# Kernel optimization log

Hardware: AMD Instinct MI355X
Metric: run time of the kernel (lower is better)

Reference implementation:

```python
import jax, jax.numpy as jnp
import numpy as np

TEMP = 0.7
EPS = 1e-6
LN_EPS = 1e-5
CAP_FACTOR = 2.0


def setup_inputs() -> dict:
    key = jax.random.key(0)
    B, S, H, E = 8, 4096, 2048, 8
    H2 = H // 2
    ks = jax.random.split(key, 3)
    x = jax.random.normal(ks[0], (B, S, H), jnp.float32)
    ln_w = jnp.ones((H,), jnp.float32)
    ln_b = jnp.zeros((H,), jnp.float32)
    # kaiming_normal_(fan_in, relu): std = sqrt(2 / fan_in)
    w1 = jax.random.normal(ks[1], (H2, H), jnp.float32) * np.float32(np.sqrt(2.0 / H))
    b1 = jnp.zeros((H2,), jnp.float32)
    w2 = jax.random.normal(ks[2], (E, H2), jnp.float32) * np.float32(np.sqrt(2.0 / H2))
    b2 = jnp.zeros((E,), jnp.float32)
    return {"x": x, "ln_w": ln_w, "ln_b": ln_b, "w1": w1, "b1": b1,
            "w2": w2, "b2": b2, "top_k": 2, "num_experts": E}


def _forward(x, ln_w, ln_b, w1, b1, w2, b2, top_k, num_experts):
    B, S, H = x.shape
    N = B * S
    # router: LayerNorm -> Linear -> GELU(exact) -> Linear
    mu = x.mean(-1, keepdims=True)
    var = jnp.mean((x - mu) ** 2, axis=-1, keepdims=True)
    h = (x - mu) * jax.lax.rsqrt(var + LN_EPS) * ln_w + ln_b
    h = jax.nn.gelu(h @ w1.T + b1, approximate=False)
    logits = h @ w2.T + b2
    ew = jnp.clip(logits / TEMP, -50.0, 50.0)  # [B,S,E]

    flat = ew.reshape(N, num_experts)
    capacity = int(CAP_FACTOR * N * top_k / num_experts)

    # top-k per token + softmax over the k selected logits, scatter into dense mask
    tk_w, tk_i = jax.lax.top_k(flat, top_k)          # [N,k]
    sm = jax.nn.softmax(tk_w, axis=-1)               # [N,k]
    rows = jnp.arange(N)[:, None]
    masks = jnp.zeros((N, num_experts), flat.dtype).at[rows, tk_i].set(sm)

    # capacity drop: per expert column, if sum of weights > capacity keep only
    # the top-`capacity` weighted tokens (extra zero-valued picks are no-ops,
    # matching the torch min(capacity, nnz) behavior).
    cols = masks.T                                   # [E,N]
    sums = cols.sum(-1)                              # [E]
    kcap = min(capacity, N)
    tv, ti = jax.lax.top_k(cols, kcap)               # [E,kcap]
    erow = jnp.arange(num_experts)[:, None]
    capped = jnp.zeros_like(cols).at[erow, ti].set(tv)
    over = sums > capacity
    cols = jnp.where(over[:, None], capped, cols)
    count = jax.lax.stop_gradient(jnp.where(over, capped.sum(-1), sums))  # buffer, no grad

    masks = cols.T
    masks = masks / jnp.maximum(masks.sum(-1, keepdims=True), EPS)

    usage = count / jnp.maximum(count.sum(), EPS)
    target = jnp.full((num_experts,), 1.0 / num_experts, usage.dtype)
    # F.kl_div(log(usage), target, reduction='batchmean') with batch dim = E
    kl = jnp.sum(target * (jnp.log(target) - jnp.log(jnp.maximum(usage, EPS)))) / num_experts
    loss = 0.01 * kl
    return ew, masks.reshape(B, S, num_experts), loss, usage


def reference(x, ln_w, ln_b, w1, b1, w2, b2, top_k, num_experts):
    return _forward(x, ln_w, ln_b, w1, b1, w2, b2, top_k, num_experts)
```

## Files before the change

kernel.cpp:

```cpp
#include <hip/hip_runtime.h>
#include <math.h>

#define NTOK 32768
#define HDIM 2048
#define H2DIM 1024
#define NE 8

#define WS_MU 0
#define WS_RS 32768
#define WS_LOGITS 65536
#define WS_SUMS (65536 + 262144)
#define WS_C1 (WS_SUMS + NE)
#define WS_C2 (WS_C1 + 1024)
#define WS_W1_BYTES 1318976ull
#define WS_NEED (WS_W1_BYTES + 8388608ull)

#define OUT_MASKS 262144
#define OUT_LOSS 524288
#define OUT_USAGE 524289

typedef _Float16 half8 __attribute__((ext_vector_type(8)));
typedef float floatx16 __attribute__((ext_vector_type(16)));

#define H_SCALE 0.03125f

__global__ __launch_bounds__(256) void w1prep_kernel(
    const float* __restrict__ w1, const float* __restrict__ ln_w,
    const float* __restrict__ ln_b, _Float16* __restrict__ w1p,
    float* __restrict__ C1, float* __restrict__ C2) {
  int idx = blockIdx.x * 256 + threadIdx.x;
  int n = idx >> 6, kc = idx & 63;
  const float4* src = (const float4*)(w1 + (size_t)n * HDIM + kc * 32);
  const float4* lwp = (const float4*)(ln_w + kc * 32);
  const float4* lbp = (const float4*)(ln_b + kc * 32);
  float wv[32], lwv[32], lbv[32];
#pragma unroll
  for (int v = 0; v < 8; ++v) {
    float4 f = src[v], g = lwp[v], h = lbp[v];
    wv[v*4+0]=f.x; wv[v*4+1]=f.y; wv[v*4+2]=f.z; wv[v*4+3]=f.w;
    lwv[v*4+0]=g.x; lwv[v*4+1]=g.y; lwv[v*4+2]=g.z; lwv[v*4+3]=g.w;
    lbv[v*4+0]=h.x; lbv[v*4+1]=h.y; lbv[v*4+2]=h.z; lbv[v*4+3]=h.w;
  }
  float c1 = 0.f, c2 = 0.f;
  _Float16 hi[32], lo[32];
#pragma unroll
  for (int v = 0; v < 32; ++v) {
    float wp = wv[v] * lwv[v];
    c1 += wp;
    c2 += lbv[v] * wv[v];
    float t = wp * 32.0f;
    hi[v] = (_Float16)t;
    lo[v] = (_Float16)((t - (float)hi[v]) * 4096.0f);
  }
  _Float16* dst = w1p + (size_t)idx * 64;
#pragma unroll
  for (int c = 0; c < 4; ++c) {
    half8 h = {hi[c*8+0],hi[c*8+1],hi[c*8+2],hi[c*8+3],hi[c*8+4],hi[c*8+5],hi[c*8+6],hi[c*8+7]};
    half8 l = {lo[c*8+0],lo[c*8+1],lo[c*8+2],lo[c*8+3],lo[c*8+4],lo[c*8+5],lo[c*8+6],lo[c*8+7]};
    *(half8*)&dst[c * 8] = h;
    *(half8*)&dst[32 + c * 8] = l;
  }
  atomicAdd(&C1[n], c1);
  atomicAdd(&C2[n], c2);
}

__global__ __launch_bounds__(256) void ln_stats_kernel(const float* __restrict__ x,
                                                       float* __restrict__ ws) {
  int g = blockIdx.x * 256 + threadIdx.x;
  if (g < NTOK * NE + NE + 2048) ws[WS_LOGITS + g] = 0.0f;

  int row = blockIdx.x * 4 + (threadIdx.x >> 6);
  int lane = threadIdx.x & 63;
  const float4* p = (const float4*)(x + (size_t)row * HDIM);
  float s = 0.f, sq = 0.f;
#pragma unroll
  for (int i = 0; i < 8; ++i) {
    float4 v = p[lane + 64 * i];
    s += (v.x + v.y) + (v.z + v.w);
    sq += (v.x * v.x + v.y * v.y) + (v.z * v.z + v.w * v.w);
  }
#pragma unroll
  for (int o = 32; o > 0; o >>= 1) {
    s += __shfl_xor(s, o);
    sq += __shfl_xor(sq, o);
  }
  if (lane == 0) {
    float m = s * (1.0f / HDIM);
    float var = fmaxf(sq * (1.0f / HDIM) - m * m, 0.0f);
    ws[WS_MU + row] = m;
    ws[WS_RS + row] = 1.0f / sqrtf(var + 1e-5f);
  }
}

#define LDB 40

__global__ __launch_bounds__(256, 3) void gemm_mfma_kernel(
    const float* __restrict__ x, const _Float16* __restrict__ w1p,
    const float* __restrict__ bias1, const float* __restrict__ w2,
    const float* __restrict__ mu, const float* __restrict__ rs,
    const float* __restrict__ C1, const float* __restrict__ C2,
    float* __restrict__ logits) {
  __shared__ _Float16 Ah[128 * LDB];
  __shared__ _Float16 Al[128 * LDB];
  __shared__ _Float16 Bh[128 * LDB];
  __shared__ _Float16 Bl[128 * LDB];

  const int tid = threadIdx.x;
  const int lin = blockIdx.x;
  const int xcd = lin & 7;
  const int jj = lin >> 3;
  const int m0 = (xcd * 32 + (jj >> 3)) * 128;
  const int n0 = (jj & 7) * 128;

  const int lane = tid & 63;
  const int wid = tid >> 6;
  const int wm = wid >> 1, wn = wid & 1;
  const int fr = lane & 31, fq = lane >> 5;

  const int am = tid >> 1, ak = (tid & 1) * 16;
  const float* xrow = x + (size_t)(m0 + am) * HDIM + ak;
  const int bn = tid >> 1, bp = tid & 1;
  const _Float16* bsrc = w1p + (size_t)(n0 + bn) * 4096 + bp * 32;
  _Float16* bdst = (bp ? Bl : Bh) + bn * LDB;
  _Float16* adst_h = Ah + am * LDB + ak;
  _Float16* adst_l = Al + am * LDB + ak;

  floatx16 acc[2][2];
#pragma unroll
  for (int i = 0; i < 2; ++i)
#pragma unroll
    for (int j = 0; j < 2; ++j)
#pragma unroll
      for (int r = 0; r < 16; ++r) acc[i][j][r] = 0.f;
  floatx16 zv;
#pragma unroll
  for (int r = 0; r < 16; ++r) zv[r] = 0.f;

  float4 xr0, xr1, xr2, xr3, br0, br1, br2, br3;
  {
    const float4* xp = (const float4*)xrow;
    xr0 = xp[0]; xr1 = xp[1]; xr2 = xp[2]; xr3 = xp[3];
    const float4* bq = (const float4*)bsrc;
    br0 = bq[0]; br1 = bq[1]; br2 = bq[2]; br3 = bq[3];
  }

  for (int kc = 0; kc < 64; ++kc) {
    float xa[16] = {xr0.x,xr0.y,xr0.z,xr0.w, xr1.x,xr1.y,xr1.z,xr1.w,
                    xr2.x,xr2.y,xr2.z,xr2.w, xr3.x,xr3.y,xr3.z,xr3.w};
    _Float16 hi[16], lo[16];
#pragma unroll
    for (int v = 0; v < 16; ++v) {
      hi[v] = (_Float16)xa[v];
      lo[v] = (_Float16)((xa[v] - (float)hi[v]) * 4096.0f);
    }

    __syncthreads();
    {
      half8 h0 = {hi[0],hi[1],hi[2],hi[3],hi[4],hi[5],hi[6],hi[7]};
      half8 h1 = {hi[8],hi[9],hi[10],hi[11],hi[12],hi[13],hi[14],hi[15]};
      half8 l0 = {lo[0],lo[1],lo[2],lo[3],lo[4],lo[5],lo[6],lo[7]};
      half8 l1 = {lo[8],lo[9],lo[10],lo[11],lo[12],lo[13],lo[14],lo[15]};
      *(half8*)adst_h = h0;
      *(half8*)(adst_h + 8) = h1;
      *(half8*)adst_l = l0;
      *(half8*)(adst_l + 8) = l1;
      float4* bd = (float4*)bdst;
      bd[0] = br0; bd[1] = br1; bd[2] = br2; bd[3] = br3;
    }
    __syncthreads();

    if (kc < 63) {
      const float4* xp = (const float4*)(xrow + (kc + 1) * 32);
      xr0 = xp[0]; xr1 = xp[1]; xr2 = xp[2]; xr3 = xp[3];
      const float4* bq = (const float4*)(bsrc + (size_t)(kc + 1) * 64);
      br0 = bq[0]; br1 = bq[1]; br2 = bq[2]; br3 = bq[3];
    }

#pragma unroll
    for (int t = 0; t < 2; ++t) {
      half8 ah[2], al[2], bh[2], bl[2];
#pragma unroll
      for (int i = 0; i < 2; ++i) {
        int off = (wm * 64 + i * 32 + fr) * LDB + t * 16 + fq * 8;
        ah[i] = *(const half8*)&Ah[off];
        al[i] = *(const half8*)&Al[off];
      }
#pragma unroll
      for (int j = 0; j < 2; ++j) {
        int off = (wn * 64 + j * 32 + fr) * LDB + t * 16 + fq * 8;
        bh[j] = *(const half8*)&Bh[off];
        bl[j] = *(const half8*)&Bl[off];
      }
#pragma unroll
      for (int i = 0; i < 2; ++i)
#pragma unroll
        for (int j = 0; j < 2; ++j) {
          acc[i][j] = __builtin_amdgcn_mfma_f32_32x32x16_f16(ah[i], bh[j], acc[i][j], 0, 0, 0);
          floatx16 tmp = __builtin_amdgcn_mfma_f32_32x32x16_f16(ah[i], bl[j], zv, 0, 0, 0);
          tmp = __builtin_amdgcn_mfma_f32_32x32x16_f16(al[i], bh[j], tmp, 0, 0, 0);
          acc[i][j] += tmp * (1.0f / 4096.0f);
        }
    }
  }

  const float inv_sqrt2 = 0.70710678118654752440f;
  const int c = fr;
  const int col0 = n0 + wn * 64 + c;
  const int col1 = col0 + 32;
  float w2r0[NE], w2r1[NE];
#pragma unroll
  for (int e = 0; e < NE; ++e) {
    w2r0[e] = w2[e * H2DIM + col0];
    w2r1[e] = w2[e * H2DIM + col1];
  }
  const float c1a = C1[col0], c1b = C1[col1];
  const float hb0 = C2[col0] + bias1[col0];
  const float hb1 = C2[col1] + bias1[col1];

#pragma unroll
  for (int i = 0; i < 2; ++i)
#pragma unroll
    for (int r = 0; r < 16; ++r) {
      int row = m0 + wm * 64 + i * 32 + (r & 3) + 8 * (r >> 2) + 4 * fq;
      float rsr = rs[row];
      float nmr = -rsr * mu[row];
      float h0 = fmaf(acc[i][0][r] * H_SCALE, rsr, fmaf(nmr, c1a, hb0));
      float h1 = fmaf(acc[i][1][r] * H_SCALE, rsr, fmaf(nmr, c1b, hb1));
      float g0 = 0.5f * h0 * (1.0f + erff(h0 * inv_sqrt2));
      float g1 = 0.5f * h1 * (1.0f + erff(h1 * inv_sqrt2));
      float pl[NE];
#pragma unroll
      for (int e = 0; e < NE; ++e) pl[e] = fmaf(g0, w2r0[e], g1 * w2r1[e]);
#pragma unroll
      for (int o = 1; o <= 16; o <<= 1)
#pragma unroll
        for (int e = 0; e < NE; ++e) pl[e] += __shfl_xor(pl[e], o);
      if (c == 0) {
#pragma unroll
        for (int e = 0; e < NE; ++e)
          atomicAdd(&logits[(size_t)row * NE + e], pl[e]);
      }
    }
}

#define BM 128
#define BN 128
#define BK 16
#define LDT 132

__global__ __launch_bounds__(256, 2) void gemm1_kernel(
    const float* __restrict__ x, const float* __restrict__ ln_w,
    const float* __restrict__ ln_b, const float* __restrict__ w1,
    const float* __restrict__ bias1, const float* __restrict__ w2,
    const float* __restrict__ mu, const float* __restrict__ rs,
    float* __restrict__ logits) {
  __shared__ float As[BK * LDT];
  __shared__ float Bs[BK * LDT];
  __shared__ float w2s[NE * BN];

  const int tid = threadIdx.x;
  const int n0 = blockIdx.x * BN;
  const int m0 = blockIdx.y * BM;

  for (int i = tid; i < NE * BN; i += 256)
    w2s[i] = w2[(size_t)(i >> 7) * H2DIM + n0 + (i & 127)];

  const int lm0 = tid >> 2;
  const int lm1 = lm0 + 64;
  const int kq = (tid & 3) * 4;
  const float* xa0 = x + (size_t)(m0 + lm0) * HDIM + kq;
  const float* xa1 = x + (size_t)(m0 + lm1) * HDIM + kq;
  const float* wb0 = w1 + (size_t)(n0 + lm0) * HDIM + kq;
  const float* wb1 = w1 + (size_t)(n0 + lm1) * HDIM + kq;
  const float mu0 = mu[m0 + lm0], rs0 = rs[m0 + lm0];
  const float mu1 = mu[m0 + lm1], rs1 = rs[m0 + lm1];

  const int tm = tid >> 4;
  const int tn = tid & 15;

  float acc[8][8] = {};

  for (int k0 = 0; k0 < HDIM; k0 += BK) {
    float4 a0 = *(const float4*)(xa0 + k0);
    float4 a1 = *(const float4*)(xa1 + k0);
    float4 b0 = *(const float4*)(wb0 + k0);
    float4 b1 = *(const float4*)(wb1 + k0);
    float4 lw = *(const float4*)(ln_w + k0 + kq);
    float4 lb = *(const float4*)(ln_b + k0 + kq);
    a0.x = (a0.x - mu0) * rs0 * lw.x + lb.x;
    a0.y = (a0.y - mu0) * rs0 * lw.y + lb.y;
    a0.z = (a0.z - mu0) * rs0 * lw.z + lb.z;
    a0.w = (a0.w - mu0) * rs0 * lw.w + lb.w;
    a1.x = (a1.x - mu1) * rs1 * lw.x + lb.x;
    a1.y = (a1.y - mu1) * rs1 * lw.y + lb.y;
    a1.z = (a1.z - mu1) * rs1 * lw.z + lb.z;
    a1.w = (a1.w - mu1) * rs1 * lw.w + lb.w;
    __syncthreads();
    As[(kq + 0) * LDT + lm0] = a0.x;
    As[(kq + 1) * LDT + lm0] = a0.y;
    As[(kq + 2) * LDT + lm0] = a0.z;
    As[(kq + 3) * LDT + lm0] = a0.w;
    As[(kq + 0) * LDT + lm1] = a1.x;
    As[(kq + 1) * LDT + lm1] = a1.y;
    As[(kq + 2) * LDT + lm1] = a1.z;
    As[(kq + 3) * LDT + lm1] = a1.w;
    Bs[(kq + 0) * LDT + lm0] = b0.x;
    Bs[(kq + 1) * LDT + lm0] = b0.y;
    Bs[(kq + 2) * LDT + lm0] = b0.z;
    Bs[(kq + 3) * LDT + lm0] = b0.w;
    Bs[(kq + 0) * LDT + lm1] = b1.x;
    Bs[(kq + 1) * LDT + lm1] = b1.y;
    Bs[(kq + 2) * LDT + lm1] = b1.z;
    Bs[(kq + 3) * LDT + lm1] = b1.w;
    __syncthreads();
#pragma unroll
    for (int kk = 0; kk < BK; ++kk) {
      float4 aLo = *(const float4*)&As[kk * LDT + tm * 8];
      float4 aHi = *(const float4*)&As[kk * LDT + tm * 8 + 4];
      float4 bLo = *(const float4*)&Bs[kk * LDT + tn * 8];
      float4 bHi = *(const float4*)&Bs[kk * LDT + tn * 8 + 4];
      float av[8] = {aLo.x, aLo.y, aLo.z, aLo.w, aHi.x, aHi.y, aHi.z, aHi.w};
      float bv[8] = {bLo.x, bLo.y, bLo.z, bLo.w, bHi.x, bHi.y, bHi.z, bHi.w};
#pragma unroll
      for (int i = 0; i < 8; ++i)
#pragma unroll
        for (int j = 0; j < 8; ++j) acc[i][j] = fmaf(av[i], bv[j], acc[i][j]);
    }
  }

  const float inv_sqrt2 = 0.70710678118654752440f;
  float bb[8];
#pragma unroll
  for (int j = 0; j < 8; ++j) bb[j] = bias1[n0 + tn * 8 + j];

#pragma unroll
  for (int i = 0; i < 8; ++i) {
    float g[8];
#pragma unroll
    for (int j = 0; j < 8; ++j) {
      float v = acc[i][j] + bb[j];
      g[j] = 0.5f * v * (1.0f + erff(v * inv_sqrt2));
    }
    float pl[NE];
#pragma unroll
    for (int e = 0; e < NE; ++e) {
      float s = 0.f;
#pragma unroll
      for (int j = 0; j < 8; ++j) s = fmaf(g[j], w2s[e * BN + tn * 8 + j], s);
      pl[e] = s;
    }
#pragma unroll
    for (int o = 1; o <= 8; o <<= 1)
#pragma unroll
      for (int e = 0; e < NE; ++e) pl[e] += __shfl_xor(pl[e], o);
    if (tn == 0) {
      int r = m0 + tm * 8 + i;
#pragma unroll
      for (int e = 0; e < NE; ++e)
        atomicAdd(&logits[(size_t)r * NE + e], pl[e]);
    }
  }
}

__global__ __launch_bounds__(256) void route_kernel(const float* __restrict__ logits,
                                                    const float* __restrict__ b2,
                                                    float* __restrict__ out,
                                                    float* __restrict__ sums) {
  __shared__ float ssum[NE];
  if (threadIdx.x < NE) ssum[threadIdx.x] = 0.f;
  __syncthreads();

  int tok = blockIdx.x * 256 + threadIdx.x;
  const float4* lp = (const float4*)(logits + (size_t)tok * NE);
  float4 l0 = lp[0], l1 = lp[1];
  float lv[NE] = {l0.x, l0.y, l0.z, l0.w, l1.x, l1.y, l1.z, l1.w};
  float ew[NE];
#pragma unroll
  for (int e = 0; e < NE; ++e) {
    float v = (lv[e] + b2[e]) / 0.7f;
    ew[e] = fminf(fmaxf(v, -50.0f), 50.0f);
  }

  int i1 = 0;
  float v1 = ew[0];
#pragma unroll
  for (int e = 1; e < NE; ++e)
    if (ew[e] > v1) { v1 = ew[e]; i1 = e; }
  int i2 = -1;
  float v2 = -1e30f;
#pragma unroll
  for (int e = 0; e < NE; ++e)
    if (e != i1 && ew[e] > v2) { v2 = ew[e]; i2 = e; }

  float t = expf(v2 - v1);
  float sm1 = 1.0f / (1.0f + t);
  float sm2 = t / (1.0f + t);
  float rsum = fmaxf(sm1 + sm2, 1e-6f);
  float m1 = sm1 / rsum, m2 = sm2 / rsum;

  float4* oew = (float4*)(out + (size_t)tok * NE);
  oew[0] = make_float4(ew[0], ew[1], ew[2], ew[3]);
  oew[1] = make_float4(ew[4], ew[5], ew[6], ew[7]);

  float mv[NE];
#pragma unroll
  for (int e = 0; e < NE; ++e)
    mv[e] = (e == i1) ? m1 : ((e == i2) ? m2 : 0.0f);
  float4* om = (float4*)(out + OUT_MASKS + (size_t)tok * NE);
  om[0] = make_float4(mv[0], mv[1], mv[2], mv[3]);
  om[1] = make_float4(mv[4], mv[5], mv[6], mv[7]);

  atomicAdd(&ssum[i1], sm1);
  atomicAdd(&ssum[i2], sm2);
  __syncthreads();
  if (threadIdx.x < NE) atomicAdd(&sums[threadIdx.x], ssum[threadIdx.x]);
}

__global__ void finalize_kernel(const float* __restrict__ sums,
                                float* __restrict__ out) {
  if (threadIdx.x != 0 || blockIdx.x != 0) return;
  float c[NE], tot = 0.f;
  for (int e = 0; e < NE; ++e) {
    c[e] = sums[e];
    tot += c[e];
  }
  float target = 1.0f / NE;
  float lt = logf(target);
  float kl = 0.f;
  for (int e = 0; e < NE; ++e) {
    float u = c[e] / fmaxf(tot, 1e-6f);
    out[OUT_USAGE + e] = u;
    kl += target * (lt - logf(fmaxf(u, 1e-6f)));
  }
  out[OUT_LOSS] = 0.01f * (kl / NE);
}

extern "C" void kernel_launch(void* const* d_in, const int* in_sizes, int n_in,
                              void* d_out, int out_size, void* d_ws, size_t ws_size,
                              hipStream_t stream) {
  const float* x = (const float*)d_in[0];
  const float* ln_w = (const float*)d_in[1];
  const float* ln_b = (const float*)d_in[2];
  const float* w1 = (const float*)d_in[3];
  const float* b1 = (const float*)d_in[4];
  const float* w2 = (const float*)d_in[5];
  const float* b2 = (const float*)d_in[6];
  float* out = (float*)d_out;
  float* ws = (float*)d_ws;
  _Float16* w1p = (_Float16*)((char*)d_ws + WS_W1_BYTES);

  const bool use_mfma = ws_size >= WS_NEED;

  ln_stats_kernel<<<NTOK / 4, 256, 0, stream>>>(x, ws);
  if (use_mfma) {
    w1prep_kernel<<<256, 256, 0, stream>>>(w1, ln_w, ln_b, w1p,
                                           ws + WS_C1, ws + WS_C2);
    gemm_mfma_kernel<<<2048, 256, 0, stream>>>(
        x, w1p, b1, w2, ws + WS_MU, ws + WS_RS, ws + WS_C1, ws + WS_C2,
        ws + WS_LOGITS);
  } else {
    gemm1_kernel<<<dim3(H2DIM / BN, NTOK / BM), 256, 0, stream>>>(
        x, ln_w, ln_b, w1, b1, w2, ws + WS_MU, ws + WS_RS, ws + WS_LOGITS);
  }
  route_kernel<<<NTOK / 256, 256, 0, stream>>>(ws + WS_LOGITS, b2, out,
                                               ws + WS_SUMS);
  finalize_kernel<<<1, 64, 0, stream>>>(ws + WS_SUMS, out);
}
```

Baseline: 1.177 ms.

## Fuse LayerNorm stats into MFMA GEMM and stream W1 via global_load_lds

Removes the separate ln_stats pass over x by accumulating per-row sum and sum-of-squares inside the GEMM K-loop, then computing mean and rstd in the epilogue from shared memory. W1 is pre-packed into an MFMA-fragment-friendly layout and loaded directly into double-buffered LDS with global_load_lds, replacing the register-staged copies. The prep kernel also zeroes the logits buffer and uses warp reductions instead of atomics for C1/C2. The fallback FP32 GEMM and the workspace-size check are dropped, so the code now assumes the workspace is large enough.

```diff
diff --git a/kernel.cpp b/kernel.cpp
--- a/kernel.cpp
+++ b/kernel.cpp
@@ -6,13 +6,11 @@
 #define H2DIM 1024
 #define NE 8
 
-#define WS_MU 0
-#define WS_RS 32768
-#define WS_LOGITS 65536
-#define WS_SUMS (65536 + 262144)
-#define WS_C1 (WS_SUMS + NE)
-#define WS_C2 (WS_C1 + 1024)
-#define WS_W1_BYTES 1318976ull
+#define WS_LOGITS 0
+#define WS_SUMS 262144
+#define WS_C1 262160
+#define WS_C2 263184
+#define WS_W1_BYTES 1057024ull
 #define WS_NEED (WS_W1_BYTES + 8388608ull)
 
 #define OUT_MASKS 262144
@@ -24,12 +22,22 @@
 
 #define H_SCALE 0.03125f
 
+#define GLDS16(g, l)                                                   \
+  __builtin_amdgcn_global_load_lds(                                    \
+      (const __attribute__((address_space(1))) void*)(g),              \
+      (__attribute__((address_space(3))) void*)(l), 16, 0, 0)
+
 __global__ __launch_bounds__(256) void w1prep_kernel(
     const float* __restrict__ w1, const float* __restrict__ ln_w,
     const float* __restrict__ ln_b, _Float16* __restrict__ w1p,
-    float* __restrict__ C1, float* __restrict__ C2) {
-  int idx = blockIdx.x * 256 + threadIdx.x;
-  int n = idx >> 6, kc = idx & 63;
+    float* __restrict__ ws) {
+  const int tid = threadIdx.x;
+  ((float4*)(ws + WS_LOGITS))[blockIdx.x * 256 + tid] =
+      make_float4(0.f, 0.f, 0.f, 0.f);
+  if (blockIdx.x == 0 && tid < NE) ws[WS_SUMS + tid] = 0.f;
+
+  const int n = blockIdx.x * 4 + (tid >> 6);
+  const int kc = tid & 63;
   const float4* src = (const float4*)(w1 + (size_t)n * HDIM + kc * 32);
   const float4* lwp = (const float4*)(ln_w + kc * 32);
   const float4* lbp = (const float4*)(ln_b + kc * 32);
@@ -52,63 +60,41 @@
     hi[v] = (_Float16)t;
     lo[v] = (_Float16)((t - (float)hi[v]) * 4096.0f);
   }
-  _Float16* dst = w1p + (size_t)idx * 64;
-#pragma unroll
-  for (int c = 0; c < 4; ++c) {
-    half8 h = {hi[c*8+0],hi[c*8+1],hi[c*8+2],hi[c*8+3],hi[c*8+4],hi[c*8+5],hi[c*8+6],hi[c*8+7]};
-    half8 l = {lo[c*8+0],lo[c*8+1],lo[c*8+2],lo[c*8+3],lo[c*8+4],lo[c*8+5],lo[c*8+6],lo[c*8+7]};
-    *(half8*)&dst[c * 8] = h;
-    *(half8*)&dst[32 + c * 8] = l;
-  }
-  atomicAdd(&C1[n], c1);
-  atomicAdd(&C2[n], c2);
-}
-
-__global__ __launch_bounds__(256) void ln_stats_kernel(const float* __restrict__ x,
-                                                       float* __restrict__ ws) {
-  int g = blockIdx.x * 256 + threadIdx.x;
-  if (g < NTOK * NE + NE + 2048) ws[WS_LOGITS + g] = 0.0f;
-
-  int row = blockIdx.x * 4 + (threadIdx.x >> 6);
-  int lane = threadIdx.x & 63;
-  const float4* p = (const float4*)(x + (size_t)row * HDIM);
-  float s = 0.f, sq = 0.f;
-#pragma unroll
-  for (int i = 0; i < 8; ++i) {
-    float4 v = p[lane + 64 * i];
-    s += (v.x + v.y) + (v.z + v.w);
-    sq += (v.x * v.x + v.y * v.y) + (v.z * v.z + v.w * v.w);
-  }
-#pragma unroll
-  for (int o = 32; o > 0; o >>= 1) {
-    s += __shfl_xor(s, o);
-    sq += __shfl_xor(sq, o);
-  }
-  if (lane == 0) {
-    float m = s * (1.0f / HDIM);
-    float var = fmaxf(sq * (1.0f / HDIM) - m * m, 0.0f);
-    ws[WS_MU + row] = m;
-    ws[WS_RS + row] = 1.0f / sqrtf(var + 1e-5f);
-  }
-}
-
-#define LDB 40
+  _Float16* dst = w1p + ((size_t)(n >> 5) * 64 + kc) * 2048;
+  const int ln8 = (n & 31) * 8;
+#pragma unroll
+  for (int st = 0; st < 2; ++st)
+#pragma unroll
+    for (int f = 0; f < 2; ++f) {
+      const int b = st * 16 + f * 8;
+      half8 h = {hi[b+0],hi[b+1],hi[b+2],hi[b+3],hi[b+4],hi[b+5],hi[b+6],hi[b+7]};
+      half8 l = {lo[b+0],lo[b+1],lo[b+2],lo[b+3],lo[b+4],lo[b+5],lo[b+6],lo[b+7]};
+      *(half8*)&dst[st * 1024 + 0 + f * 256 + ln8] = h;
+      *(half8*)&dst[st * 1024 + 512 + f * 256 + ln8] = l;
+    }
+#pragma unroll
+  for (int o = 1; o < 64; o <<= 1) {
+    c1 += __shfl_xor(c1, o);
+    c2 += __shfl_xor(c2, o);
+  }
+  if (kc == 0) {
+    ws[WS_C1 + n] = c1;
+    ws[WS_C2 + n] = c2;
+  }
+}
 
 __global__ __launch_bounds__(256, 3) void gemm_mfma_kernel(
     const float* __restrict__ x, const _Float16* __restrict__ w1p,
     const float* __restrict__ bias1, const float* __restrict__ w2,
-    const float* __restrict__ mu, const float* __restrict__ rs,
     const float* __restrict__ C1, const float* __restrict__ C2,
     float* __restrict__ logits) {
-  __shared__ _Float16 Ah[128 * LDB];
-  __shared__ _Float16 Al[128 * LDB];
-  __shared__ _Float16 Bh[128 * LDB];
-  __shared__ _Float16 Bl[128 * LDB];
+  __shared__ _Float16 Abuf[8192];
+  __shared__ _Float16 Bbuf[2][8192];
+  __shared__ float sRow[128], sqRow[128];
 
   const int tid = threadIdx.x;
   const int lin = blockIdx.x;
-  const int xcd = lin & 7;
-  const int jj = lin >> 3;
+  const int xcd = lin & 7, jj = lin >> 3;
   const int m0 = (xcd * 32 + (jj >> 3)) * 128;
   const int n0 = (jj & 7) * 128;
 
@@ -117,13 +103,12 @@
   const int wm = wid >> 1, wn = wid & 1;
   const int fr = lane & 31, fq = lane >> 5;
 
-  const int am = tid >> 1, ak = (tid & 1) * 16;
-  const float* xrow = x + (size_t)(m0 + am) * HDIM + ak;
-  const int bn = tid >> 1, bp = tid & 1;
-  const _Float16* bsrc = w1p + (size_t)(n0 + bn) * 4096 + bp * 32;
-  _Float16* bdst = (bp ? Bl : Bh) + bn * LDB;
-  _Float16* adst_h = Ah + am * LDB + ak;
-  _Float16* adst_l = Al + am * LDB + ak;
+  const int am = tid >> 1, st = tid & 1;
+  const float* xrow = x + (size_t)(m0 + am) * HDIM + st * 16;
+  _Float16* adst = Abuf + (am >> 5) * 2048 + st * 1024 + (am & 31) * 8;
+
+  const _Float16* bsrc =
+      w1p + ((size_t)((n0 >> 5) + wid) * 64) * 2048 + lane * 8;
 
   floatx16 acc[2][2];
 #pragma unroll
@@ -136,20 +121,27 @@
 #pragma unroll
   for (int r = 0; r < 16; ++r) zv[r] = 0.f;
 
-  float4 xr0, xr1, xr2, xr3, br0, br1, br2, br3;
+  float s = 0.f, sq = 0.f;
+  float4 xr0, xr1, xr2, xr3;
   {
+    _Float16* bd = &Bbuf[0][wid * 2048];
+    GLDS16(bsrc + 0, bd + 0);
+    GLDS16(bsrc + 512, bd + 512);
+    GLDS16(bsrc + 1024, bd + 1024);
+    GLDS16(bsrc + 1536, bd + 1536);
     const float4* xp = (const float4*)xrow;
     xr0 = xp[0]; xr1 = xp[1]; xr2 = xp[2]; xr3 = xp[3];
-    const float4* bq = (const float4*)bsrc;
-    br0 = bq[0]; br1 = bq[1]; br2 = bq[2]; br3 = bq[3];
   }
 
   for (int kc = 0; kc < 64; ++kc) {
+    const int p = kc & 1;
     float xa[16] = {xr0.x,xr0.y,xr0.z,xr0.w, xr1.x,xr1.y,xr1.z,xr1.w,
                     xr2.x,xr2.y,xr2.z,xr2.w, xr3.x,xr3.y,xr3.z,xr3.w};
     _Float16 hi[16], lo[16];
 #pragma unroll
     for (int v = 0; v < 16; ++v) {
+      s += xa[v];
+      sq = fmaf(xa[v], xa[v], sq);
       hi[v] = (_Float16)xa[v];
       lo[v] = (_Float16)((xa[v] - (float)hi[v]) * 4096.0f);
     }
@@ -160,20 +152,22 @@
       half8 h1 = {hi[8],hi[9],hi[10],hi[11],hi[12],hi[13],hi[14],hi[15]};
       half8 l0 = {lo[0],lo[1],lo[2],lo[3],lo[4],lo[5],lo[6],lo[7]};
       half8 l1 = {lo[8],lo[9],lo[10],lo[11],lo[12],lo[13],lo[14],lo[15]};
-      *(half8*)adst_h = h0;
-      *(half8*)(adst_h + 8) = h1;
-      *(half8*)adst_l = l0;
-      *(half8*)(adst_l + 8) = l1;
-      float4* bd = (float4*)bdst;
-      bd[0] = br0; bd[1] = br1; bd[2] = br2; bd[3] = br3;
+      *(half8*)(adst + 0) = h0;
+      *(half8*)(adst + 256) = h1;
+      *(half8*)(adst + 512) = l0;
+      *(half8*)(adst + 768) = l1;
     }
     __syncthreads();
 
     if (kc < 63) {
+      const _Float16* bs = bsrc + (size_t)(kc + 1) * 2048;
+      _Float16* bd = &Bbuf[p ^ 1][wid * 2048];
+      GLDS16(bs + 0, bd + 0);
+      GLDS16(bs + 512, bd + 512);
+      GLDS16(bs + 1024, bd + 1024);
+      GLDS16(bs + 1536, bd + 1536);
       const float4* xp = (const float4*)(xrow + (kc + 1) * 32);
       xr0 = xp[0]; xr1 = xp[1]; xr2 = xp[2]; xr3 = xp[3];
-      const float4* bq = (const float4*)(bsrc + (size_t)(kc + 1) * 64);
-      br0 = bq[0]; br1 = bq[1]; br2 = bq[2]; br3 = bq[3];
     }
 
 #pragma unroll
@@ -181,15 +175,15 @@
       half8 ah[2], al[2], bh[2], bl[2];
 #pragma unroll
       for (int i = 0; i < 2; ++i) {
-        int off = (wm * 64 + i * 32 + fr) * LDB + t * 16 + fq * 8;
-        ah[i] = *(const half8*)&Ah[off];
-        al[i] = *(const half8*)&Al[off];
+        const int off = (wm * 2 + i) * 2048 + t * 1024 + lane * 8;
+        ah[i] = *(const half8*)&Abuf[off];
+        al[i] = *(const half8*)&Abuf[off + 512];
       }
 #pragma unroll
       for (int j = 0; j < 2; ++j) {
-        int off = (wn * 64 + j * 32 + fr) * LDB + t * 16 + fq * 8;
-        bh[j] = *(const half8*)&Bh[off];
-        bl[j] = *(const half8*)&Bl[off];
+        const int off = (wn * 2 + j) * 2048 + t * 1024 + lane * 8;
+        bh[j] = *(const half8*)&Bbuf[p][off];
+        bl[j] = *(const half8*)&Bbuf[p][off + 512];
       }
 #pragma unroll
       for (int i = 0; i < 2; ++i)
@@ -203,6 +197,11 @@
     }
   }
 
+  s += __shfl_xor(s, 1);
+  sq += __shfl_xor(sq, 1);
+  if (st == 0) { sRow[am] = s; sqRow[am] = sq; }
+  __syncthreads();
+
   const float inv_sqrt2 = 0.70710678118654752440f;
   const int c = fr;
   const int col0 = n0 + wn * 64 + c;
@@ -221,9 +220,12 @@
   for (int i = 0; i < 2; ++i)
 #pragma unroll
     for (int r = 0; r < 16; ++r) {
-      int row = m0 + wm * 64 + i * 32 + (r & 3) + 8 * (r >> 2) + 4 * fq;
-      float rsr = rs[row];
-      float nmr = -rsr * mu[row];
+      const int lr = wm * 64 + i * 32 + (r & 3) + 8 * (r >> 2) + 4 * fq;
+      const float mu_r = sRow[lr] * (1.0f / HDIM);
+      const float var =
+          fmaxf(sqRow[lr] * (1.0f / HDIM) - mu_r * mu_r, 0.0f);
+      const float rsr = 1.0f / sqrtf(var + 1e-5f);
+      const float nmr = -rsr * mu_r;
       float h0 = fmaf(acc[i][0][r] * H_SCALE, rsr, fmaf(nmr, c1a, hb0));
       float h1 = fmaf(acc[i][1][r] * H_SCALE, rsr, fmaf(nmr, c1b, hb1));
       float g0 = 0.5f * h0 * (1.0f + erff(h0 * inv_sqrt2));
@@ -236,130 +238,12 @@
 #pragma unroll
         for (int e = 0; e < NE; ++e) pl[e] += __shfl_xor(pl[e], o);
       if (c == 0) {
+        const int row = m0 + lr;
 #pragma unroll
         for (int e = 0; e < NE; ++e)
           atomicAdd(&logits[(size_t)row * NE + e], pl[e]);
       }
     }
-}
-
-#define BM 128
-#define BN 128
-#define BK 16
-#define LDT 132
-
-__global__ __launch_bounds__(256, 2) void gemm1_kernel(
-    const float* __restrict__ x, const float* __restrict__ ln_w,
-    const float* __restrict__ ln_b, const float* __restrict__ w1,
-    const float* __restrict__ bias1, const float* __restrict__ w2,
-    const float* __restrict__ mu, const float* __restrict__ rs,
-    float* __restrict__ logits) {
-  __shared__ float As[BK * LDT];
-  __shared__ float Bs[BK * LDT];
-  __shared__ float w2s[NE * BN];
-
-  const int tid = threadIdx.x;
-  const int n0 = blockIdx.x * BN;
-  const int m0 = blockIdx.y * BM;
-
-  for (int i = tid; i < NE * BN; i += 256)
-    w2s[i] = w2[(size_t)(i >> 7) * H2DIM + n0 + (i & 127)];
-
-  const int lm0 = tid >> 2;
-  const int lm1 = lm0 + 64;
-  const int kq = (tid & 3) * 4;
-  const float* xa0 = x + (size_t)(m0 + lm0) * HDIM + kq;
-  const float* xa1 = x + (size_t)(m0 + lm1) * HDIM + kq;
-  const float* wb0 = w1 + (size_t)(n0 + lm0) * HDIM + kq;
-  const float* wb1 = w1 + (size_t)(n0 + lm1) * HDIM + kq;
-  const float mu0 = mu[m0 + lm0], rs0 = rs[m0 + lm0];
-  const float mu1 = mu[m0 + lm1], rs1 = rs[m0 + lm1];
-
-  const int tm = tid >> 4;
-  const int tn = tid & 15;
-
-  float acc[8][8] = {};
-
-  for (int k0 = 0; k0 < HDIM; k0 += BK) {
-    float4 a0 = *(const float4*)(xa0 + k0);
-    float4 a1 = *(const float4*)(xa1 + k0);
-    float4 b0 = *(const float4*)(wb0 + k0);
-    float4 b1 = *(const float4*)(wb1 + k0);
-    float4 lw = *(const float4*)(ln_w + k0 + kq);
-    float4 lb = *(const float4*)(ln_b + k0 + kq);
-    a0.x = (a0.x - mu0) * rs0 * lw.x + lb.x;
-    a0.y = (a0.y - mu0) * rs0 * lw.y + lb.y;
-    a0.z = (a0.z - mu0) * rs0 * lw.z + lb.z;
-    a0.w = (a0.w - mu0) * rs0 * lw.w + lb.w;
-    a1.x = (a1.x - mu1) * rs1 * lw.x + lb.x;
-    a1.y = (a1.y - mu1) * rs1 * lw.y + lb.y;
-    a1.z = (a1.z - mu1) * rs1 * lw.z + lb.z;
-    a1.w = (a1.w - mu1) * rs1 * lw.w + lb.w;
-    __syncthreads();
-    As[(kq + 0) * LDT + lm0] = a0.x;
-    As[(kq + 1) * LDT + lm0] = a0.y;
-    As[(kq + 2) * LDT + lm0] = a0.z;
-    As[(kq + 3) * LDT + lm0] = a0.w;
-    As[(kq + 0) * LDT + lm1] = a1.x;
-    As[(kq + 1) * LDT + lm1] = a1.y;
-    As[(kq + 2) * LDT + lm1] = a1.z;
-    As[(kq + 3) * LDT + lm1] = a1.w;
-    Bs[(kq + 0) * LDT + lm0] = b0.x;
-    Bs[(kq + 1) * LDT + lm0] = b0.y;
-    Bs[(kq + 2) * LDT + lm0] = b0.z;
-    Bs[(kq + 3) * LDT + lm0] = b0.w;
-    Bs[(kq + 0) * LDT + lm1] = b1.x;
-    Bs[(kq + 1) * LDT + lm1] = b1.y;
-    Bs[(kq + 2) * LDT + lm1] = b1.z;
-    Bs[(kq + 3) * LDT + lm1] = b1.w;
-    __syncthreads();
-#pragma unroll
-    for (int kk = 0; kk < BK; ++kk) {
-      float4 aLo = *(const float4*)&As[kk * LDT + tm * 8];
-      float4 aHi = *(const float4*)&As[kk * LDT + tm * 8 + 4];
-      float4 bLo = *(const float4*)&Bs[kk * LDT + tn * 8];
-      float4 bHi = *(const float4*)&Bs[kk * LDT + tn * 8 + 4];
-      float av[8] = {aLo.x, aLo.y, aLo.z, aLo.w, aHi.x, aHi.y, aHi.z, aHi.w};
-      float bv[8] = {bLo.x, bLo.y, bLo.z, bLo.w, bHi.x, bHi.y, bHi.z, bHi.w};
-#pragma unroll
-      for (int i = 0; i < 8; ++i)
-#pragma unroll
-        for (int j = 0; j < 8; ++j) acc[i][j] = fmaf(av[i], bv[j], acc[i][j]);
-    }
-  }
-
-  const float inv_sqrt2 = 0.70710678118654752440f;
-  float bb[8];
-#pragma unroll
-  for (int j = 0; j < 8; ++j) bb[j] = bias1[n0 + tn * 8 + j];
-
-#pragma unroll
-  for (int i = 0; i < 8; ++i) {
-    float g[8];
-#pragma unroll
-    for (int j = 0; j < 8; ++j) {
-      float v = acc[i][j] + bb[j];
-      g[j] = 0.5f * v * (1.0f + erff(v * inv_sqrt2));
-    }
-    float pl[NE];
-#pragma unroll
-    for (int e = 0; e < NE; ++e) {
-      float s = 0.f;
-#pragma unroll
-      for (int j = 0; j < 8; ++j) s = fmaf(g[j], w2s[e * BN + tn * 8 + j], s);
-      pl[e] = s;
-    }
-#pragma unroll
-    for (int o = 1; o <= 8; o <<= 1)
-#pragma unroll
-      for (int e = 0; e < NE; ++e) pl[e] += __shfl_xor(pl[e], o);
-    if (tn == 0) {
-      int r = m0 + tm * 8 + i;
-#pragma unroll
-      for (int e = 0; e < NE; ++e)
-        atomicAdd(&logits[(size_t)r * NE + e], pl[e]);
-    }
-  }
 }
 
 __global__ __launch_bounds__(256) void route_kernel(const float* __restrict__ logits,
@@ -448,20 +332,11 @@
   float* out = (float*)d_out;
   float* ws = (float*)d_ws;
   _Float16* w1p = (_Float16*)((char*)d_ws + WS_W1_BYTES);
-
-  const bool use_mfma = ws_size >= WS_NEED;
-
-  ln_stats_kernel<<<NTOK / 4, 256, 0, stream>>>(x, ws);
-  if (use_mfma) {
-    w1prep_kernel<<<256, 256, 0, stream>>>(w1, ln_w, ln_b, w1p,
-                                           ws + WS_C1, ws + WS_C2);
-    gemm_mfma_kernel<<<2048, 256, 0, stream>>>(
-        x, w1p, b1, w2, ws + WS_MU, ws + WS_RS, ws + WS_C1, ws + WS_C2,
-        ws + WS_LOGITS);
-  } else {
-    gemm1_kernel<<<dim3(H2DIM / BN, NTOK / BM), 256, 0, stream>>>(
-        x, ln_w, ln_b, w1, b1, w2, ws + WS_MU, ws + WS_RS, ws + WS_LOGITS);
-  }
+  (void)ws_size;
+
+  w1prep_kernel<<<256, 256, 0, stream>>>(w1, ln_w, ln_b, w1p, ws);
+  gemm_mfma_kernel<<<2048, 256, 0, stream>>>(
+      x, w1p, b1, w2, ws + WS_C1, ws + WS_C2, ws + WS_LOGITS);
   route_kernel<<<NTOK / 256, 256, 0, stream>>>(ws + WS_LOGITS, b2, out,
                                                ws + WS_SUMS);
   finalize_kernel<<<1, 64, 0, stream>>>(ws + WS_SUMS, out);
```

Result: faster. 1.142 ms (-3.0%).
